# Kernel optimization log

Hardware: AMD Instinct MI355X
Metric: run time of the kernel (lower is better)

## Reference

```python
import jax, jax.numpy as jnp
import numpy as np

H = 16  # num heads

def setup_inputs() -> dict:
    key = jax.random.key(0)
    k1, k2, k3 = jax.random.split(key, 3)
    B, L, D = 2, 2048, 1024
    x = jax.random.normal(k1, (B, L, D), dtype=jnp.float32)
    # torch Linear weight is [out,in]; we store transposed [in,out] so y = x @ W
    w_qkv = jax.random.normal(k2, (D, 3 * D), dtype=jnp.float32) * (D ** -0.5)
    w_proj = jax.random.normal(k3, (D, D), dtype=jnp.float32) * (D ** -0.5)
    return {"x": x, "w_qkv": w_qkv, "w_proj": w_proj, "num_prefix_tokens": 256}

def _prefix_causal_mask(L: int, M: int):
    # True = masked. Strict upper triangle (causal), then text rows (M:) may
    # see ALL prefix columns (:M).
    mask = jnp.triu(jnp.ones((L, L), dtype=bool), k=1)
    mask = mask.at[M:, :M].set(False)
    return mask

def reference(x, w_qkv, w_proj, num_prefix_tokens):
    B, L, D = x.shape
    d = D // H
    scale = d ** -0.5
    qkv = (x @ w_qkv).reshape(B, L, 3, H, d)
    q = jnp.transpose(qkv[:, :, 0], (0, 2, 1, 3))  # [B,H,L,d]
    k = jnp.transpose(qkv[:, :, 1], (0, 2, 1, 3))
    v = jnp.transpose(qkv[:, :, 2], (0, 2, 1, 3))
    logits = jnp.einsum("bhqd,bhkd->bhqk", q, k) * scale  # [B,H,L,L]
    mask = _prefix_causal_mask(L, num_prefix_tokens)
    logits = jnp.where(mask[None, None], -jnp.inf, logits)
    attn = jax.nn.softmax(logits, axis=-1)
    out = jnp.einsum("bhqk,bhkd->bhqd", attn, v)  # [B,H,L,d]
    out = jnp.transpose(out, (0, 2, 1, 3)).reshape(B, L, D)
    return out @ w_proj
```

## Files before the change

kernel.cpp:

```cpp
#include <hip/hip_runtime.h>
#include <hip/hip_bf16.h>

#define BATCH   2
#define L_SEQ   2048
#define DMODEL  1024
#define NHEADS  16
#define DHEAD   64
#define SEG     (BATCH*NHEADS*L_SEQ*DHEAD)

typedef __attribute__((ext_vector_type(8)))  short bf16x8;
typedef __attribute__((ext_vector_type(4)))  float f32x4;
typedef __attribute__((ext_vector_type(16))) float f32x16;

__device__ __forceinline__ unsigned short f2b(float f) {
    unsigned int u = __float_as_uint(f);
    return (unsigned short)((u + 0x7FFFu + ((u >> 16) & 1u)) >> 16);
}
__device__ __forceinline__ unsigned int pk2(float a, float b) {
    __hip_bfloat162 h = __float22bfloat162_rn(make_float2(a, b));
    return *(unsigned int*)&h;
}
__device__ __forceinline__ void glds16(const unsigned short* g, unsigned short* l) {
    __builtin_amdgcn_global_load_lds(
        (const __attribute__((address_space(1))) unsigned int*)g,
        (__attribute__((address_space(3))) unsigned int*)l, 16, 0, 0);
}

__global__ __launch_bounds__(256)
void cast_bf16(const float* __restrict__ in, unsigned short* __restrict__ out, int n) {
    int i = (blockIdx.x * 256 + threadIdx.x) * 4;
    if (i < n) {
        float4 f = *(const float4*)&in[i];
        ushort4 o;
        o.x = f2b(f.x); o.y = f2b(f.y); o.z = f2b(f.z); o.w = f2b(f.w);
        *(ushort4*)&out[i] = o;
    }
}

__global__ __launch_bounds__(256)
void transpose_cast(const float* __restrict__ in, unsigned short* __restrict__ out,
                    int K, int N) {
    __shared__ unsigned short T[64][65];
    const int k0 = blockIdx.y * 64, n0 = blockIdx.x * 64;
    const int t = threadIdx.x;
    const int r = t >> 4, c4 = (t & 15) * 4;
#pragma unroll
    for (int rep = 0; rep < 4; ++rep) {
        int kk = rep * 16 + r;
        float4 f = *(const float4*)&in[(size_t)(k0 + kk) * N + n0 + c4];
        T[kk][c4 + 0] = f2b(f.x);
        T[kk][c4 + 1] = f2b(f.y);
        T[kk][c4 + 2] = f2b(f.z);
        T[kk][c4 + 3] = f2b(f.w);
    }
    __syncthreads();
#pragma unroll
    for (int rep = 0; rep < 4; ++rep) {
        int nn = rep * 16 + r;
        ushort4 o;
        o.x = T[c4 + 0][nn];
        o.y = T[c4 + 1][nn];
        o.z = T[c4 + 2][nn];
        o.w = T[c4 + 3][nn];
        *(ushort4*)&out[(size_t)(n0 + nn) * K + k0 + c4] = o;
    }
}

template <int MODE>
__global__ __launch_bounds__(256)
void gemm_bf16(const unsigned short* __restrict__ A, const unsigned short* __restrict__ Bt,
               float* __restrict__ Cf, unsigned short* __restrict__ Cb,
               int M, int K, int N) {
    __shared__ unsigned short Asm[128 * 64];
    __shared__ unsigned short Bsm[128 * 64];

    const int t = threadIdx.x;
    const int lane = t & 63, wave = t >> 6;
    const int quad = lane >> 4, l16 = lane & 15;
    const int wm = (wave >> 1) * 64, wn = (wave & 1) * 64;
    const int id = blockIdx.y * gridDim.x + blockIdx.x;
    const int seq = id >> 3;
    const int m0 = ((id & 7) * 4 + (seq & 3)) * 128;
    const int n0 = (seq >> 2) * 128;

    const int gsw = (lane & 7) ^ (lane >> 3);
    const unsigned short* ga[4];
    const unsigned short* gb[4];
    unsigned short* la[4];
    unsigned short* lb[4];
#pragma unroll
    for (int i = 0; i < 4; ++i) {
        int row = wave * 32 + i * 8 + (lane >> 3);
        ga[i] = &A[(size_t)(m0 + row) * K + gsw * 8];
        gb[i] = &Bt[(size_t)(n0 + row) * K + gsw * 8];
        la[i] = &Asm[(wave * 32 + i * 8) * 64];
        lb[i] = &Bsm[(wave * 32 + i * 8) * 64];
    }
    const int sx = l16 & 7;

    f32x4 acc[4][4];
#pragma unroll
    for (int i = 0; i < 4; ++i)
#pragma unroll
        for (int j = 0; j < 4; ++j)
#pragma unroll
            for (int r = 0; r < 4; ++r) acc[i][j][r] = 0.0f;

    for (int k0 = 0; k0 < K; k0 += 64) {
        __syncthreads();
#pragma unroll
        for (int i = 0; i < 4; ++i) {
            glds16(ga[i] + k0, la[i]);
            glds16(gb[i] + k0, lb[i]);
        }
        __syncthreads();
#pragma unroll
        for (int s = 0; s < 2; ++s) {
            bf16x8 af[4], bfr[4];
#pragma unroll
            for (int i = 0; i < 4; ++i)
                af[i] = *(const bf16x8*)&Asm[(wm + i * 16 + l16) * 64 + ((4 * s + quad) ^ sx) * 8];
#pragma unroll
            for (int j = 0; j < 4; ++j)
                bfr[j] = *(const bf16x8*)&Bsm[(wn + j * 16 + l16) * 64 + ((4 * s + quad) ^ sx) * 8];
#pragma unroll
            for (int i = 0; i < 4; ++i)
#pragma unroll
                for (int j = 0; j < 4; ++j)
                    acc[i][j] = __builtin_amdgcn_mfma_f32_16x16x32_bf16(af[i], bfr[j], acc[i][j], 0, 0, 0);
        }
    }

    if (MODE == 0) {
#pragma unroll
        for (int i = 0; i < 4; ++i)
#pragma unroll
            for (int r = 0; r < 4; ++r) {
                int row = m0 + wm + i * 16 + quad * 4 + r;
#pragma unroll
                for (int j = 0; j < 4; ++j) {
                    int col = n0 + wn + j * 16 + l16;
                    Cf[(size_t)row * N + col] = acc[i][j][r];
                }
            }
    } else {
        const float qscale = 0.1803368801111244f;
#pragma unroll
        for (int j = 0; j < 4; ++j) {
            int n = n0 + wn + j * 16 + l16;
            int s = n >> 10, h = (n >> 6) & 15, dd = n & 63;
            float scl = (s == 0) ? qscale : 1.0f;
#pragma unroll
            for (int i = 0; i < 4; ++i)
#pragma unroll
                for (int r = 0; r < 4; ++r) {
                    int row = m0 + wm + i * 16 + quad * 4 + r;
                    int b = row >> 11, lpos = row & (L_SEQ - 1);
                    size_t dst = (size_t)s * SEG +
                                 (((size_t)(b * NHEADS + h) * L_SEQ + lpos) * DHEAD) + dd;
                    Cb[dst] = f2b(acc[i][j][r] * scl);
                }
        }
    }
}

__global__ __launch_bounds__(256)
void gemm_vT(const unsigned short* __restrict__ A, const unsigned short* __restrict__ Bt,
             unsigned short* __restrict__ Vt, int M, int K) {
    __shared__ unsigned short Asm[128 * 64];
    __shared__ unsigned short Bsm[128 * 64];

    const int t = threadIdx.x;
    const int lane = t & 63, wave = t >> 6;
    const int quad = lane >> 4, l16 = lane & 15;
    const int wm = (wave >> 1) * 64, wn = (wave & 1) * 64;
    const int id = blockIdx.y * gridDim.x + blockIdx.x;
    const int seq = id >> 3;
    const int m0 = ((id & 7) * 4 + (seq & 3)) * 128;
    const int n0 = (seq >> 2) * 128;

    const int gsw = (lane & 7) ^ (lane >> 3);
    const unsigned short* ga[4];
    const unsigned short* gb[4];
    unsigned short* la[4];
    unsigned short* lb[4];
#pragma unroll
    for (int i = 0; i < 4; ++i) {
        int row = wave * 32 + i * 8 + (lane >> 3);
        ga[i] = &A[(size_t)(m0 + row) * K + gsw * 8];
        gb[i] = &Bt[(size_t)(n0 + row) * K + gsw * 8];
        la[i] = &Asm[(wave * 32 + i * 8) * 64];
        lb[i] = &Bsm[(wave * 32 + i * 8) * 64];
    }
    const int sx = l16 & 7;

    f32x4 acc[4][4];
#pragma unroll
    for (int i = 0; i < 4; ++i)
#pragma unroll
        for (int j = 0; j < 4; ++j)
#pragma unroll
            for (int r = 0; r < 4; ++r) acc[i][j][r] = 0.0f;

    for (int k0 = 0; k0 < K; k0 += 64) {
        __syncthreads();
#pragma unroll
        for (int i = 0; i < 4; ++i) {
            glds16(ga[i] + k0, la[i]);
            glds16(gb[i] + k0, lb[i]);
        }
        __syncthreads();
#pragma unroll
        for (int s = 0; s < 2; ++s) {
            bf16x8 af[4], bfr[4];
#pragma unroll
            for (int i = 0; i < 4; ++i)
                af[i] = *(const bf16x8*)&Asm[(wm + i * 16 + l16) * 64 + ((4 * s + quad) ^ sx) * 8];
#pragma unroll
            for (int j = 0; j < 4; ++j)
                bfr[j] = *(const bf16x8*)&Bsm[(wn + j * 16 + l16) * 64 + ((4 * s + quad) ^ sx) * 8];
#pragma unroll
            for (int i = 0; i < 4; ++i)
#pragma unroll
                for (int j = 0; j < 4; ++j)
                    acc[i][j] = __builtin_amdgcn_mfma_f32_16x16x32_bf16(bfr[j], af[i], acc[i][j], 0, 0, 0);
        }
    }

#pragma unroll
    for (int j = 0; j < 4; ++j)
#pragma unroll
        for (int r = 0; r < 4; ++r) {
            int f = n0 + wn + j * 16 + quad * 4 + r;
            int h = f >> 6, dd = f & 63;
#pragma unroll
            for (int i = 0; i < 4; ++i) {
                int token = m0 + wm + i * 16 + l16;
                int b = token >> 11, lpos = token & (L_SEQ - 1);
                size_t dst = (((size_t)(b * NHEADS + h) * DHEAD + dd) * L_SEQ) + lpos;
                Vt[dst] = f2b(acc[i][j][r]);
            }
        }
}

__global__ __launch_bounds__(256)
void attn_mfma(const unsigned short* __restrict__ Qg, const unsigned short* __restrict__ Kg,
               const unsigned short* __restrict__ Vg, unsigned short* __restrict__ Ao) {
    __shared__ unsigned short Ksm[64 * 64];
    __shared__ unsigned short Vsm[64 * 64];
    __shared__ unsigned short Psm[4 * 32 * 64];

    const int t = threadIdx.x;
    const int lane = t & 63, wave = t >> 6;
    const int l31 = lane & 31, hi = lane >> 5, l7 = lane & 7;
    const int bh = blockIdx.x & 31;
    const int Qt = 15 - (blockIdx.x >> 5);
    const int b = bh >> 4, h = bh & 15;
    const size_t qkbase = (size_t)bh * L_SEQ * DHEAD;
    const size_t vbase  = (size_t)bh * DHEAD * L_SEQ;
    const int wq0 = Qt * 128 + wave * 32;
    const int nkt = 2 * Qt + 2;

    bf16x8 bq[4];
#pragma unroll
    for (int ks = 0; ks < 4; ++ks)
        bq[ks] = *(const bf16x8*)&Qg[qkbase + (size_t)(wq0 + l31) * DHEAD + ks * 16 + hi * 8];

    const int r0 = t >> 3, c0 = t & 7;
    const int gsw = c0 ^ (r0 & 7);
    const int ls0 = r0 * 64 + c0 * 8, ls1 = (r0 + 32) * 64 + c0 * 8;

    unsigned short* Pw = Psm + wave * 32 * 64;

    f32x16 O0, O1;
#pragma unroll
    for (int r = 0; r < 16; ++r) { O0[r] = 0.0f; O1[r] = 0.0f; }
    float rs = 0.0f;

    bf16x8 gk0 = *(const bf16x8*)&Kg[qkbase + (size_t)r0 * DHEAD + gsw * 8];
    bf16x8 gk1 = *(const bf16x8*)&Kg[qkbase + (size_t)(r0 + 32) * DHEAD + gsw * 8];
    bf16x8 gv0 = *(const bf16x8*)&Vg[vbase + (size_t)r0 * L_SEQ + gsw * 8];
    bf16x8 gv1 = *(const bf16x8*)&Vg[vbase + (size_t)(r0 + 32) * L_SEQ + gsw * 8];

    for (int kt = 0; kt < nkt; ++kt) {
        __syncthreads();
        *(bf16x8*)&Ksm[ls0] = gk0;
        *(bf16x8*)&Ksm[ls1] = gk1;
        *(bf16x8*)&Vsm[ls0] = gv0;
        *(bf16x8*)&Vsm[ls1] = gv1;
        if (kt + 1 < nkt) {
            const int kn = (kt + 1) * 64;
            gk0 = *(const bf16x8*)&Kg[qkbase + (size_t)(kn + r0) * DHEAD + gsw * 8];
            gk1 = *(const bf16x8*)&Kg[qkbase + (size_t)(kn + r0 + 32) * DHEAD + gsw * 8];
            gv0 = *(const bf16x8*)&Vg[vbase + (size_t)r0 * L_SEQ + kn + gsw * 8];
            gv1 = *(const bf16x8*)&Vg[vbase + (size_t)(r0 + 32) * L_SEQ + kn + gsw * 8];
        }
        __syncthreads();

        const int k0g = kt * 64;
        if (k0g <= wq0 + 31) {
            f32x16 ST[2];
#pragma unroll
            for (int kh = 0; kh < 2; ++kh) {
#pragma unroll
                for (int r = 0; r < 16; ++r) ST[kh][r] = 0.0f;
#pragma unroll
                for (int ks = 0; ks < 4; ++ks) {
                    bf16x8 a = *(const bf16x8*)&Ksm[(kh * 32 + l31) * 64 + (((ks * 2 + hi) ^ l7) * 8)];
                    ST[kh] = __builtin_amdgcn_mfma_f32_32x32x16_bf16(a, bq[ks], ST[kh], 0, 0, 0);
                }
            }

            if (k0g + 63 > wq0) {
                const int qg = wq0 + l31;
#pragma unroll
                for (int kh = 0; kh < 2; ++kh)
#pragma unroll
                    for (int r = 0; r < 16; ++r) {
                        int keyg = k0g + kh * 32 + (r & 3) + 8 * (r >> 2) + 4 * hi;
                        if (keyg > qg) ST[kh][r] = -1e30f;
                    }
            }

#pragma unroll
            for (int kh = 0; kh < 2; ++kh)
#pragma unroll
                for (int g = 0; g < 4; ++g) {
                    float p0 = __builtin_amdgcn_exp2f(ST[kh][4 * g + 0]);
                    float p1 = __builtin_amdgcn_exp2f(ST[kh][4 * g + 1]);
                    float p2 = __builtin_amdgcn_exp2f(ST[kh][4 * g + 2]);
                    float p3 = __builtin_amdgcn_exp2f(ST[kh][4 * g + 3]);
                    rs += (p0 + p1) + (p2 + p3);
                    *(uint2*)&Pw[l31 * 64 + (((kh * 4 + g) ^ l7) * 8) + hi * 4] =
                        make_uint2(pk2(p0, p1), pk2(p2, p3));
                }

#pragma unroll
            for (int ks = 0; ks < 4; ++ks) {
                bf16x8 pa = *(const bf16x8*)&Pw[l31 * 64 + (((ks * 2 + hi) ^ l7) * 8)];
                bf16x8 v0 = *(const bf16x8*)&Vsm[(l31) * 64 + (((ks * 2 + hi) ^ l7) * 8)];
                bf16x8 v1 = *(const bf16x8*)&Vsm[(32 + l31) * 64 + (((ks * 2 + hi) ^ l7) * 8)];
                O0 = __builtin_amdgcn_mfma_f32_32x32x16_bf16(pa, v0, O0, 0, 0, 0);
                O1 = __builtin_amdgcn_mfma_f32_32x32x16_bf16(pa, v1, O1, 0, 0, 0);
            }
        }
    }

    rs += __shfl_xor(rs, 32, 64);
    float linv = 1.0f / rs;
    float lf[16];
#pragma unroll
    for (int r = 0; r < 16; ++r) {
        int qloc = (r & 3) + 8 * (r >> 2) + 4 * hi;
        lf[r] = __shfl(linv, qloc, 32);
    }
#pragma unroll
    for (int r = 0; r < 16; ++r) {
        int qloc = (r & 3) + 8 * (r >> 2) + 4 * hi;
        int token = wq0 + qloc;
        size_t ob = ((size_t)(b * L_SEQ + token)) * DMODEL + h * DHEAD;
        Ao[ob + l31]      = f2b(O0[r] * lf[r]);
        Ao[ob + 32 + l31] = f2b(O1[r] * lf[r]);
    }
}

extern "C" void kernel_launch(void* const* d_in, const int* in_sizes, int n_in,
                              void* d_out, int out_size, void* d_ws, size_t ws_size,
                              hipStream_t stream) {
    const float* x      = (const float*)d_in[0];
    const float* w_qkv  = (const float*)d_in[1];
    const float* w_proj = (const float*)d_in[2];
    float* out = (float*)d_out;

    unsigned short* ws     = (unsigned short*)d_ws;
    unsigned short* xb     = ws;
    unsigned short* wqkvT  = xb + 4194304;
    unsigned short* wprojT = wqkvT + 3145728;
    unsigned short* qkv    = wprojT + 1048576;
    unsigned short* ao     = qkv + 3 * (size_t)SEG;

    const int M = BATCH * L_SEQ;

    cast_bf16<<<4096, 256, 0, stream>>>(x, xb, M * DMODEL);
    transpose_cast<<<dim3(48, 16), 256, 0, stream>>>(w_qkv, wqkvT, DMODEL, 3 * DMODEL);
    transpose_cast<<<dim3(16, 16), 256, 0, stream>>>(w_proj, wprojT, DMODEL, DMODEL);

    gemm_bf16<1><<<dim3(16, 32), 256, 0, stream>>>(xb, wqkvT, nullptr, qkv, M, DMODEL, 2048);
    gemm_vT<<<dim3(8, 32), 256, 0, stream>>>(xb, wqkvT + 2048 * DMODEL, qkv + 2 * (size_t)SEG,
                                             M, DMODEL);

    attn_mfma<<<512, 256, 0, stream>>>(qkv, qkv + SEG, qkv + 2 * (size_t)SEG, ao);

    gemm_bf16<0><<<dim3(8, 32), 256, 0, stream>>>(ao, wprojT, out, nullptr, M, DMODEL, DMODEL);
}
```

Before: 194.0 us.

## Fuse prep kernels, merge QKV and V GEMMs, split attention keys across waves

Merges the three cast and transpose launches into one prep kernel. Merges the QK and V-transposed GEMMs into one launch that picks the output layout per block. Drops the grouped block-index swizzle in favour of plain row and column indexing. Reworks attention to use 64-query tiles with 1024 blocks, where wave pairs split each 128-key strip and their partial outputs are combined through shared memory. This cuts launch count and aims for better occupancy and load balance in attention, at the cost of extra shared memory, an added reduction step, and possibly worse L2 locality in the GEMMs.

```diff
diff --git a/kernel.cpp b/kernel.cpp
--- a/kernel.cpp
+++ b/kernel.cpp
@@ -26,23 +26,11 @@
         (__attribute__((address_space(3))) unsigned int*)l, 16, 0, 0);
 }
 
-__global__ __launch_bounds__(256)
-void cast_bf16(const float* __restrict__ in, unsigned short* __restrict__ out, int n) {
-    int i = (blockIdx.x * 256 + threadIdx.x) * 4;
-    if (i < n) {
-        float4 f = *(const float4*)&in[i];
-        ushort4 o;
-        o.x = f2b(f.x); o.y = f2b(f.y); o.z = f2b(f.z); o.w = f2b(f.w);
-        *(ushort4*)&out[i] = o;
-    }
-}
-
-__global__ __launch_bounds__(256)
-void transpose_cast(const float* __restrict__ in, unsigned short* __restrict__ out,
-                    int K, int N) {
+__device__ __forceinline__ void tcast64(const float* __restrict__ in,
+                                        unsigned short* __restrict__ out,
+                                        int K, int N, int bx, int by, int t) {
     __shared__ unsigned short T[64][65];
-    const int k0 = blockIdx.y * 64, n0 = blockIdx.x * 64;
-    const int t = threadIdx.x;
+    const int k0 = by * 64, n0 = bx * 64;
     const int r = t >> 4, c4 = (t & 15) * 4;
 #pragma unroll
     for (int rep = 0; rep < 4; ++rep) {
@@ -66,11 +54,29 @@
     }
 }
 
-template <int MODE>
 __global__ __launch_bounds__(256)
-void gemm_bf16(const unsigned short* __restrict__ A, const unsigned short* __restrict__ Bt,
-               float* __restrict__ Cf, unsigned short* __restrict__ Cb,
-               int M, int K, int N) {
+void prep(const float* __restrict__ x, const float* __restrict__ wqkv,
+          const float* __restrict__ wproj, unsigned short* __restrict__ xb,
+          unsigned short* __restrict__ wqkvT, unsigned short* __restrict__ wprojT) {
+    const int id = blockIdx.x, t = threadIdx.x;
+    if (id < 4096) {
+        int i = id * 1024 + t * 4;
+        float4 f = *(const float4*)&x[i];
+        ushort4 o;
+        o.x = f2b(f.x); o.y = f2b(f.y); o.z = f2b(f.z); o.w = f2b(f.w);
+        *(ushort4*)&xb[i] = o;
+    } else if (id < 4864) {
+        int lid = id - 4096;
+        tcast64(wqkv, wqkvT, DMODEL, 3 * DMODEL, lid % 48, lid / 48, t);
+    } else {
+        int lid = id - 4864;
+        tcast64(wproj, wprojT, DMODEL, DMODEL, lid & 15, lid >> 4, t);
+    }
+}
+
+__global__ __launch_bounds__(256)
+void gemm_qkv(const unsigned short* __restrict__ A, const unsigned short* __restrict__ Bt,
+              unsigned short* __restrict__ Cb) {
     __shared__ unsigned short Asm[128 * 64];
     __shared__ unsigned short Bsm[128 * 64];
 
@@ -78,10 +84,9 @@
     const int lane = t & 63, wave = t >> 6;
     const int quad = lane >> 4, l16 = lane & 15;
     const int wm = (wave >> 1) * 64, wn = (wave & 1) * 64;
-    const int id = blockIdx.y * gridDim.x + blockIdx.x;
-    const int seq = id >> 3;
-    const int m0 = ((id & 7) * 4 + (seq & 3)) * 128;
-    const int n0 = (seq >> 2) * 128;
+    const int m0 = blockIdx.y * 128, n0 = blockIdx.x * 128;
+    const int K = DMODEL;
+    const bool vrole = (n0 >= 2048);
 
     const int gsw = (lane & 7) ^ (lane >> 3);
     const unsigned short* ga[4];
@@ -123,27 +128,23 @@
 #pragma unroll
             for (int j = 0; j < 4; ++j)
                 bfr[j] = *(const bf16x8*)&Bsm[(wn + j * 16 + l16) * 64 + ((4 * s + quad) ^ sx) * 8];
-#pragma unroll
-            for (int i = 0; i < 4; ++i)
-#pragma unroll
-                for (int j = 0; j < 4; ++j)
-                    acc[i][j] = __builtin_amdgcn_mfma_f32_16x16x32_bf16(af[i], bfr[j], acc[i][j], 0, 0, 0);
-        }
-    }
-
-    if (MODE == 0) {
-#pragma unroll
-        for (int i = 0; i < 4; ++i)
-#pragma unroll
-            for (int r = 0; r < 4; ++r) {
-                int row = m0 + wm + i * 16 + quad * 4 + r;
-#pragma unroll
-                for (int j = 0; j < 4; ++j) {
-                    int col = n0 + wn + j * 16 + l16;
-                    Cf[(size_t)row * N + col] = acc[i][j][r];
-                }
-            }
-    } else {
+            if (!vrole) {
+#pragma unroll
+                for (int i = 0; i < 4; ++i)
+#pragma unroll
+                    for (int j = 0; j < 4; ++j)
+                        acc[i][j] = __builtin_amdgcn_mfma_f32_16x16x32_bf16(af[i], bfr[j], acc[i][j], 0, 0, 0);
+            } else {
+#pragma unroll
+                for (int i = 0; i < 4; ++i)
+#pragma unroll
+                    for (int j = 0; j < 4; ++j)
+                        acc[i][j] = __builtin_amdgcn_mfma_f32_16x16x32_bf16(bfr[j], af[i], acc[i][j], 0, 0, 0);
+            }
+        }
+    }
+
+    if (!vrole) {
         const float qscale = 0.1803368801111244f;
 #pragma unroll
         for (int j = 0; j < 4; ++j) {
@@ -161,12 +162,28 @@
                     Cb[dst] = f2b(acc[i][j][r] * scl);
                 }
         }
+    } else {
+#pragma unroll
+        for (int j = 0; j < 4; ++j)
+#pragma unroll
+            for (int r = 0; r < 4; ++r) {
+                int f = (n0 - 2048) + wn + j * 16 + quad * 4 + r;
+                int h = f >> 6, dd = f & 63;
+#pragma unroll
+                for (int i = 0; i < 4; ++i) {
+                    int token = m0 + wm + i * 16 + l16;
+                    int b = token >> 11, lpos = token & (L_SEQ - 1);
+                    size_t dst = 2 * (size_t)SEG +
+                                 (((size_t)(b * NHEADS + h) * DHEAD + dd) * L_SEQ) + lpos;
+                    Cb[dst] = f2b(acc[i][j][r]);
+                }
+            }
     }
 }
 
 __global__ __launch_bounds__(256)
-void gemm_vT(const unsigned short* __restrict__ A, const unsigned short* __restrict__ Bt,
-             unsigned short* __restrict__ Vt, int M, int K) {
+void gemm_proj(const unsigned short* __restrict__ A, const unsigned short* __restrict__ Bt,
+               float* __restrict__ Cf) {
     __shared__ unsigned short Asm[128 * 64];
     __shared__ unsigned short Bsm[128 * 64];
 
@@ -174,10 +191,8 @@
     const int lane = t & 63, wave = t >> 6;
     const int quad = lane >> 4, l16 = lane & 15;
     const int wm = (wave >> 1) * 64, wn = (wave & 1) * 64;
-    const int id = blockIdx.y * gridDim.x + blockIdx.x;
-    const int seq = id >> 3;
-    const int m0 = ((id & 7) * 4 + (seq & 3)) * 128;
-    const int n0 = (seq >> 2) * 128;
+    const int m0 = blockIdx.y * 128, n0 = blockIdx.x * 128;
+    const int K = DMODEL, N = DMODEL;
 
     const int gsw = (lane & 7) ^ (lane >> 3);
     const unsigned short* ga[4];
@@ -223,52 +238,48 @@
             for (int i = 0; i < 4; ++i)
 #pragma unroll
                 for (int j = 0; j < 4; ++j)
-                    acc[i][j] = __builtin_amdgcn_mfma_f32_16x16x32_bf16(bfr[j], af[i], acc[i][j], 0, 0, 0);
-        }
-    }
-
-#pragma unroll
-    for (int j = 0; j < 4; ++j)
+                    acc[i][j] = __builtin_amdgcn_mfma_f32_16x16x32_bf16(af[i], bfr[j], acc[i][j], 0, 0, 0);
+        }
+    }
+
+#pragma unroll
+    for (int i = 0; i < 4; ++i)
 #pragma unroll
         for (int r = 0; r < 4; ++r) {
-            int f = n0 + wn + j * 16 + quad * 4 + r;
-            int h = f >> 6, dd = f & 63;
-#pragma unroll
-            for (int i = 0; i < 4; ++i) {
-                int token = m0 + wm + i * 16 + l16;
-                int b = token >> 11, lpos = token & (L_SEQ - 1);
-                size_t dst = (((size_t)(b * NHEADS + h) * DHEAD + dd) * L_SEQ) + lpos;
-                Vt[dst] = f2b(acc[i][j][r]);
-            }
+            int row = m0 + wm + i * 16 + quad * 4 + r;
+#pragma unroll
+            for (int j = 0; j < 4; ++j)
+                Cf[(size_t)row * N + n0 + wn + j * 16 + l16] = acc[i][j][r];
         }
 }
 
 __global__ __launch_bounds__(256)
 void attn_mfma(const unsigned short* __restrict__ Qg, const unsigned short* __restrict__ Kg,
                const unsigned short* __restrict__ Vg, unsigned short* __restrict__ Ao) {
-    __shared__ unsigned short Ksm[64 * 64];
-    __shared__ unsigned short Vsm[64 * 64];
+    __shared__ unsigned short Ksm[128 * 64];
+    __shared__ unsigned short Vsm[64 * 128];
     __shared__ unsigned short Psm[4 * 32 * 64];
 
     const int t = threadIdx.x;
     const int lane = t & 63, wave = t >> 6;
-    const int l31 = lane & 31, hi = lane >> 5, l7 = lane & 7;
+    const int l31 = lane & 31, hi = lane >> 5;
     const int bh = blockIdx.x & 31;
-    const int Qt = 15 - (blockIdx.x >> 5);
+    const int Qt = 31 - (blockIdx.x >> 5);
+    const int q0 = Qt * 64;
+    const int qh = wave & 1, kp = wave >> 1;
+    const int wq0 = q0 + qh * 32;
+    const int nstrip = (Qt >> 1) + 1;
     const int b = bh >> 4, h = bh & 15;
     const size_t qkbase = (size_t)bh * L_SEQ * DHEAD;
     const size_t vbase  = (size_t)bh * DHEAD * L_SEQ;
-    const int wq0 = Qt * 128 + wave * 32;
-    const int nkt = 2 * Qt + 2;
 
     bf16x8 bq[4];
 #pragma unroll
     for (int ks = 0; ks < 4; ++ks)
         bq[ks] = *(const bf16x8*)&Qg[qkbase + (size_t)(wq0 + l31) * DHEAD + ks * 16 + hi * 8];
 
-    const int r0 = t >> 3, c0 = t & 7;
-    const int gsw = c0 ^ (r0 & 7);
-    const int ls0 = r0 * 64 + c0 * 8, ls1 = (r0 + 32) * 64 + c0 * 8;
+    const int kc0 = t & 7,  kr0 = (t >> 3) * 4;
+    const int vc0 = t & 15, vd0 = (t >> 4) * 4;
 
     unsigned short* Pw = Psm + wave * 32 * 64;
 
@@ -277,28 +288,32 @@
     for (int r = 0; r < 16; ++r) { O0[r] = 0.0f; O1[r] = 0.0f; }
     float rs = 0.0f;
 
-    bf16x8 gk0 = *(const bf16x8*)&Kg[qkbase + (size_t)r0 * DHEAD + gsw * 8];
-    bf16x8 gk1 = *(const bf16x8*)&Kg[qkbase + (size_t)(r0 + 32) * DHEAD + gsw * 8];
-    bf16x8 gv0 = *(const bf16x8*)&Vg[vbase + (size_t)r0 * L_SEQ + gsw * 8];
-    bf16x8 gv1 = *(const bf16x8*)&Vg[vbase + (size_t)(r0 + 32) * L_SEQ + gsw * 8];
-
-    for (int kt = 0; kt < nkt; ++kt) {
-        __syncthreads();
-        *(bf16x8*)&Ksm[ls0] = gk0;
-        *(bf16x8*)&Ksm[ls1] = gk1;
-        *(bf16x8*)&Vsm[ls0] = gv0;
-        *(bf16x8*)&Vsm[ls1] = gv1;
-        if (kt + 1 < nkt) {
-            const int kn = (kt + 1) * 64;
-            gk0 = *(const bf16x8*)&Kg[qkbase + (size_t)(kn + r0) * DHEAD + gsw * 8];
-            gk1 = *(const bf16x8*)&Kg[qkbase + (size_t)(kn + r0 + 32) * DHEAD + gsw * 8];
-            gv0 = *(const bf16x8*)&Vg[vbase + (size_t)r0 * L_SEQ + kn + gsw * 8];
-            gv1 = *(const bf16x8*)&Vg[vbase + (size_t)(r0 + 32) * L_SEQ + kn + gsw * 8];
-        }
-        __syncthreads();
-
-        const int k0g = kt * 64;
-        if (k0g <= wq0 + 31) {
+    bf16x8 gk[4], gv[4];
+#pragma unroll
+    for (int i = 0; i < 4; ++i) {
+        gk[i] = *(const bf16x8*)&Kg[qkbase + (size_t)(kr0 + i) * DHEAD + kc0 * 8];
+        gv[i] = *(const bf16x8*)&Vg[vbase + (size_t)(vd0 + i) * L_SEQ + vc0 * 8];
+    }
+
+    for (int s = 0; s < nstrip; ++s) {
+        __syncthreads();
+#pragma unroll
+        for (int i = 0; i < 4; ++i) {
+            *(bf16x8*)&Ksm[(kc0 * 128 + ((kr0 + i) ^ kc0)) * 8] = gk[i];
+            *(bf16x8*)&Vsm[(vc0 * 64 + ((vd0 + i) ^ vc0)) * 8] = gv[i];
+        }
+        if (s + 1 < nstrip) {
+            const int kn = (s + 1) * 128;
+#pragma unroll
+            for (int i = 0; i < 4; ++i) {
+                gk[i] = *(const bf16x8*)&Kg[qkbase + (size_t)(kn + kr0 + i) * DHEAD + kc0 * 8];
+                gv[i] = *(const bf16x8*)&Vg[vbase + (size_t)(vd0 + i) * L_SEQ + kn + vc0 * 8];
+            }
+        }
+        __syncthreads();
+
+        const int keybase = s * 128 + kp * 64;
+        if (keybase <= wq0 + 31) {
             f32x16 ST[2];
 #pragma unroll
             for (int kh = 0; kh < 2; ++kh) {
@@ -306,18 +321,20 @@
                 for (int r = 0; r < 16; ++r) ST[kh][r] = 0.0f;
 #pragma unroll
                 for (int ks = 0; ks < 4; ++ks) {
-                    bf16x8 a = *(const bf16x8*)&Ksm[(kh * 32 + l31) * 64 + (((ks * 2 + hi) ^ l7) * 8)];
+                    const int c = ks * 2 + hi;
+                    const int rk = kp * 64 + kh * 32 + l31;
+                    bf16x8 a = *(const bf16x8*)&Ksm[(c * 128 + (rk ^ c)) * 8];
                     ST[kh] = __builtin_amdgcn_mfma_f32_32x32x16_bf16(a, bq[ks], ST[kh], 0, 0, 0);
                 }
             }
 
-            if (k0g + 63 > wq0) {
+            if (keybase + 63 > wq0) {
                 const int qg = wq0 + l31;
 #pragma unroll
                 for (int kh = 0; kh < 2; ++kh)
 #pragma unroll
                     for (int r = 0; r < 16; ++r) {
-                        int keyg = k0g + kh * 32 + (r & 3) + 8 * (r >> 2) + 4 * hi;
+                        int keyg = keybase + kh * 32 + (r & 3) + 8 * (r >> 2) + 4 * hi;
                         if (keyg > qg) ST[kh][r] = -1e30f;
                     }
             }
@@ -331,15 +348,18 @@
                     float p2 = __builtin_amdgcn_exp2f(ST[kh][4 * g + 2]);
                     float p3 = __builtin_amdgcn_exp2f(ST[kh][4 * g + 3]);
                     rs += (p0 + p1) + (p2 + p3);
-                    *(uint2*)&Pw[l31 * 64 + (((kh * 4 + g) ^ l7) * 8) + hi * 4] =
+                    const int c = kh * 4 + g;
+                    *(uint2*)&Pw[(c * 32 + (l31 ^ c)) * 8 + hi * 4] =
                         make_uint2(pk2(p0, p1), pk2(p2, p3));
                 }
 
 #pragma unroll
             for (int ks = 0; ks < 4; ++ks) {
-                bf16x8 pa = *(const bf16x8*)&Pw[l31 * 64 + (((ks * 2 + hi) ^ l7) * 8)];
-                bf16x8 v0 = *(const bf16x8*)&Vsm[(l31) * 64 + (((ks * 2 + hi) ^ l7) * 8)];
-                bf16x8 v1 = *(const bf16x8*)&Vsm[(32 + l31) * 64 + (((ks * 2 + hi) ^ l7) * 8)];
+                const int cp = ks * 2 + hi;
+                const int cv = kp * 8 + ks * 2 + hi;
+                bf16x8 pa = *(const bf16x8*)&Pw[(cp * 32 + (l31 ^ cp)) * 8];
+                bf16x8 v0 = *(const bf16x8*)&Vsm[(cv * 64 + (l31 ^ cv)) * 8];
+                bf16x8 v1 = *(const bf16x8*)&Vsm[(cv * 64 + ((32 + l31) ^ cv)) * 8];
                 O0 = __builtin_amdgcn_mfma_f32_32x32x16_bf16(pa, v0, O0, 0, 0, 0);
                 O1 = __builtin_amdgcn_mfma_f32_32x32x16_bf16(pa, v1, O1, 0, 0, 0);
             }
@@ -347,20 +367,39 @@
     }
 
     rs += __shfl_xor(rs, 32, 64);
-    float linv = 1.0f / rs;
-    float lf[16];
-#pragma unroll
-    for (int r = 0; r < 16; ++r) {
-        int qloc = (r & 3) + 8 * (r >> 2) + 4 * hi;
-        lf[r] = __shfl(linv, qloc, 32);
-    }
-#pragma unroll
-    for (int r = 0; r < 16; ++r) {
-        int qloc = (r & 3) + 8 * (r >> 2) + 4 * hi;
-        int token = wq0 + qloc;
-        size_t ob = ((size_t)(b * L_SEQ + token)) * DMODEL + h * DHEAD;
-        Ao[ob + l31]      = f2b(O0[r] * lf[r]);
-        Ao[ob + 32 + l31] = f2b(O1[r] * lf[r]);
+
+    __syncthreads();
+    float* Oex = (float*)Ksm;
+    float* Rex = (float*)Vsm;
+    if (kp == 1) {
+#pragma unroll
+        for (int r = 0; r < 16; ++r) {
+            int qloc = (r & 3) + 8 * (r >> 2) + 4 * hi;
+            Oex[qh * 2048 + qloc * 64 + l31]      = O0[r];
+            Oex[qh * 2048 + qloc * 64 + 32 + l31] = O1[r];
+        }
+        if (hi == 0) Rex[qh * 32 + l31] = rs;
+    }
+    __syncthreads();
+    if (kp == 0) {
+        float rs_tot = rs + Rex[qh * 32 + l31];
+        float linv = 1.0f / rs_tot;
+        float lf[16];
+#pragma unroll
+        for (int r = 0; r < 16; ++r) {
+            int qloc = (r & 3) + 8 * (r >> 2) + 4 * hi;
+            O0[r] += Oex[qh * 2048 + qloc * 64 + l31];
+            O1[r] += Oex[qh * 2048 + qloc * 64 + 32 + l31];
+            lf[r] = __shfl(linv, qloc, 32);
+        }
+#pragma unroll
+        for (int r = 0; r < 16; ++r) {
+            int qloc = (r & 3) + 8 * (r >> 2) + 4 * hi;
+            int token = wq0 + qloc;
+            size_t ob = ((size_t)(b * L_SEQ + token)) * DMODEL + h * DHEAD;
+            Ao[ob + l31]      = f2b(O0[r] * lf[r]);
+            Ao[ob + 32 + l31] = f2b(O1[r] * lf[r]);
+        }
     }
 }
 
@@ -379,17 +418,11 @@
     unsigned short* qkv    = wprojT + 1048576;
     unsigned short* ao     = qkv + 3 * (size_t)SEG;
 
-    const int M = BATCH * L_SEQ;
-
-    cast_bf16<<<4096, 256, 0, stream>>>(x, xb, M * DMODEL);
-    transpose_cast<<<dim3(48, 16), 256, 0, stream>>>(w_qkv, wqkvT, DMODEL, 3 * DMODEL);
-    transpose_cast<<<dim3(16, 16), 256, 0, stream>>>(w_proj, wprojT, DMODEL, DMODEL);
-
-    gemm_bf16<1><<<dim3(16, 32), 256, 0, stream>>>(xb, wqkvT, nullptr, qkv, M, DMODEL, 2048);
-    gemm_vT<<<dim3(8, 32), 256, 0, stream>>>(xb, wqkvT + 2048 * DMODEL, qkv + 2 * (size_t)SEG,
-                                             M, DMODEL);
-
-    attn_mfma<<<512, 256, 0, stream>>>(qkv, qkv + SEG, qkv + 2 * (size_t)SEG, ao);
-
-    gemm_bf16<0><<<dim3(8, 32), 256, 0, stream>>>(ao, wprojT, out, nullptr, M, DMODEL, DMODEL);
-}
+    prep<<<5120, 256, 0, stream>>>(x, w_qkv, w_proj, xb, wqkvT, wprojT);
+
+    gemm_qkv<<<dim3(24, 32), 256, 0, stream>>>(xb, wqkvT, qkv);
+
+    attn_mfma<<<1024, 256, 0, stream>>>(qkv, qkv + SEG, qkv + 2 * (size_t)SEG, ao);
+
+    gemm_proj<<<dim3(8, 32), 256, 0, stream>>>(ao, wprojT, out);
+}
```

Result: faster. 179.2 us (-7.6%).
